# Performance work log

Hardware: AMD Instinct MI355X
Metric: run time of the kernel (lower is better)

## Reference

```python
import jax, jax.numpy as jnp
import numpy as np

H, C = 4, 32  # heads, per-head out_channels; hidden = H*C = 128


def _gatv2(x, Wl, bl, Wr, br, att, b, src, dst):
    """One PyG GATv2Conv layer (concat=True, add_self_loops=False, slope=0.2)."""
    N = x.shape[0]
    xl = (x @ Wl + bl).reshape(N, H, C)  # source transform (messages)
    xr = (x @ Wr + br).reshape(N, H, C)  # target transform
    msg = xl[src]                         # [E,H,C] gather per edge
    e = jax.nn.leaky_relu(msg + xr[dst], 0.2)
    a = jnp.einsum('ehc,hc->eh', e, att)  # [E,H] attention logits
    # segment softmax over incoming edges of each target node
    amax = jax.ops.segment_max(a, dst, num_segments=N)
    a = jnp.exp(a - amax[dst])
    denom = jax.ops.segment_sum(a, dst, num_segments=N)
    a = a / (denom[dst] + 1e-16)
    out = jax.ops.segment_sum(a[..., None] * msg, dst, num_segments=N)  # [N,H,C]
    return out.reshape(N, H * C) + b


def setup_inputs() -> dict:
    key = jax.random.key(0)
    ks = jax.random.split(key, 16)
    N, E, F = 50000, 800000, H * C
    s = 1.0 / np.sqrt(F)
    inp = {
        'x': jax.random.normal(ks[0], (N, F), dtype=jnp.float32),
        'edge_index': jax.random.randint(ks[1], (2, E), 0, N, dtype=jnp.int32),
    }
    names = ['Wl1', 'Wr1', 'Wl2', 'Wr2']
    for i, n in enumerate(names):
        inp[n] = jax.random.normal(ks[2 + i], (F, F), dtype=jnp.float32) * s
    inp['bl1'] = jnp.zeros((F,), jnp.float32)
    inp['br1'] = jnp.zeros((F,), jnp.float32)
    inp['bl2'] = jnp.zeros((F,), jnp.float32)
    inp['br2'] = jnp.zeros((F,), jnp.float32)
    inp['att1'] = jax.random.normal(ks[6], (H, C), dtype=jnp.float32) * s
    inp['att2'] = jax.random.normal(ks[7], (H, C), dtype=jnp.float32) * s
    inp['b1'] = jnp.zeros((F,), jnp.float32)
    inp['b2'] = jnp.zeros((F,), jnp.float32)
    return inp


def reference(x, edge_index, Wl1, bl1, Wr1, br1, att1, b1,
              Wl2, bl2, Wr2, br2, att2, b2):
    src, dst = edge_index[0], edge_index[1]
    h = jax.nn.relu(_gatv2(x, Wl1, bl1, Wr1, br1, att1, b1, src, dst))
    out = _gatv2(h, Wl2, bl2, Wr2, br2, att2, b2, src, dst)
    return out
```

## Files before the change

kernel.cpp:

```cpp
#include <hip/hip_runtime.h>
#include <hip/hip_bf16.h>
#include <hip/hip_fp16.h>
#include <float.h>

#define F 128
#define HEADS 4
#define CPH 32

#define NB 512
#define BSHIFT 7
#define G 64

using f16x8 = __attribute__((ext_vector_type(8))) _Float16;
using f32x4 = __attribute__((ext_vector_type(4))) float;


__global__ __launch_bounds__(1024) void bucket_hist_kernel(
    const int* __restrict__ dst, int* __restrict__ counts, int E, int chunk)
{
    __shared__ int hist[NB];
    int blk = blockIdx.x;
    for (int b = threadIdx.x; b < NB; b += 1024) hist[b] = 0;
    __syncthreads();
    int e0 = blk * chunk, e1 = min(e0 + chunk, E);
    for (int e = e0 + threadIdx.x; e < e1; e += 1024)
        atomicAdd(&hist[dst[e] >> BSHIFT], 1);
    __syncthreads();
    for (int b = threadIdx.x; b < NB; b += 1024)
        counts[b * G + blk] = hist[b];
}

__global__ __launch_bounds__(1024) void scan1_kernel(const int* __restrict__ in,
                                                     int* __restrict__ excl,
                                                     int* __restrict__ bsums, int n) {
    __shared__ int tmp[1024];
    int i = blockIdx.x * 1024 + threadIdx.x;
    int v = (i < n) ? in[i] : 0;
    tmp[threadIdx.x] = v;
    __syncthreads();
    for (int o = 1; o < 1024; o <<= 1) {
        int a = (threadIdx.x >= o) ? tmp[threadIdx.x - o] : 0;
        __syncthreads();
        tmp[threadIdx.x] += a;
        __syncthreads();
    }
    if (i < n) excl[i] = tmp[threadIdx.x] - v;
    if (threadIdx.x == 1023) bsums[blockIdx.x] = tmp[1023];
}

__global__ __launch_bounds__(1024) void scan2_kernel(int* __restrict__ bsums, int nb) {
    __shared__ int tmp[1024];
    int v = (threadIdx.x < nb) ? bsums[threadIdx.x] : 0;
    tmp[threadIdx.x] = v;
    __syncthreads();
    for (int o = 1; o < 1024; o <<= 1) {
        int a = (threadIdx.x >= o) ? tmp[threadIdx.x - o] : 0;
        __syncthreads();
        tmp[threadIdx.x] += a;
        __syncthreads();
    }
    if (threadIdx.x < nb) bsums[threadIdx.x] = tmp[threadIdx.x] - v;
}

__global__ __launch_bounds__(1024) void addback_kernel(const int* __restrict__ excl,
                                                       const int* __restrict__ bsums,
                                                       int* __restrict__ offsets, int n) {
    int i = blockIdx.x * 1024 + threadIdx.x;
    if (i < n) offsets[i] = excl[i] + bsums[i >> 10];
}

__global__ __launch_bounds__(1024) void bucket_scatter_kernel(
    const int* __restrict__ src, const int* __restrict__ dst,
    const int* __restrict__ offsets, uint2* __restrict__ pairs, int E, int chunk)
{
    __shared__ int curs[NB];
    int blk = blockIdx.x;
    for (int b = threadIdx.x; b < NB; b += 1024) curs[b] = offsets[b * G + blk];
    __syncthreads();
    int e0 = blk * chunk, e1 = min(e0 + chunk, E);
    for (int e = e0 + threadIdx.x; e < e1; e += 1024) {
        int d = dst[e];
        int pos = atomicAdd(&curs[d >> BSHIFT], 1);
        pairs[pos] = make_uint2((unsigned)src[e], (unsigned)d);
    }
}

__global__ __launch_bounds__(256) void bucket_csr_kernel(
    const uint2* __restrict__ pairs, const int* __restrict__ offsets,
    int* __restrict__ row_ptr, int* __restrict__ srcs, int N, int E)
{
    int b = blockIdx.x;
    int seg0 = offsets[b * G];
    int seg1 = (b < NB - 1) ? offsets[(b + 1) * G] : E;
    __shared__ int hist[128], curs[128];
    if (threadIdx.x < 128) hist[threadIdx.x] = 0;
    __syncthreads();
    for (int e = seg0 + threadIdx.x; e < seg1; e += 256)
        atomicAdd(&hist[pairs[e].y & 127], 1);
    __syncthreads();
    int v = (threadIdx.x < 128) ? hist[threadIdx.x] : 0;
    if (threadIdx.x < 128) curs[threadIdx.x] = v;
    __syncthreads();
    for (int o = 1; o < 128; o <<= 1) {
        int a = 0;
        if (threadIdx.x < 128 && threadIdx.x >= o) a = curs[threadIdx.x - o];
        __syncthreads();
        if (threadIdx.x < 128) curs[threadIdx.x] += a;
        __syncthreads();
    }
    int excl = (threadIdx.x < 128) ? curs[threadIdx.x] - v : 0;
    __syncthreads();
    if (threadIdx.x < 128) {
        int node = b * 128 + threadIdx.x;
        if (node <= N) row_ptr[node] = seg0 + excl;
        curs[threadIdx.x] = excl;
    }
    __syncthreads();
    for (int e = seg0 + threadIdx.x; e < seg1; e += 256) {
        uint2 p = pairs[e];
        int pos = seg0 + atomicAdd(&curs[p.y & 127], 1);
        srcs[pos] = (int)p.x;
    }
}

__global__ void convw_kernel(const float* __restrict__ W0, const float* __restrict__ W1,
                             const float* __restrict__ W2, const float* __restrict__ W3,
                             _Float16* __restrict__ T0, _Float16* __restrict__ T1,
                             _Float16* __restrict__ T2, _Float16* __restrict__ T3) {
    int m   = blockIdx.x >> 6;
    int tid = (blockIdx.x & 63) * 256 + threadIdx.x;
    int n = tid >> 7, k = tid & 127;
    const float* W = m == 0 ? W0 : m == 1 ? W1 : m == 2 ? W2 : W3;
    _Float16*    T = m == 0 ? T0 : m == 1 ? T1 : m == 2 ? T2 : T3;
    T[tid] = (_Float16)W[k * F + n];
}


template<int A_FP32>
__global__ __launch_bounds__(256) void mfma_gemm_kernel(
    const void* __restrict__ Xin,
    const _Float16* __restrict__ Wlt, const float* __restrict__ bl,
    const _Float16* __restrict__ Wrt, const float* __restrict__ br,
    _Float16* __restrict__ xl, float* __restrict__ xr, int N)
{
    const int m = blockIdx.y;
    const _Float16* Wt = m ? Wrt : Wlt;

    __shared__ f16x8 Ws[F * 17];
    for (int i = threadIdx.x; i < F * 16; i += 256) {
        int row = i >> 4, g = i & 15;
        Ws[row * 17 + g] = ((const f16x8*)Wt)[i];
    }
    __syncthreads();

    const int wid  = threadIdx.x >> 6;
    const int lane = threadIdx.x & 63;
    const int row0 = blockIdx.x * 64 + wid * 16;
    const int arow = lane & 15;
    const int g    = lane >> 4;

    int xrow = row0 + arow;
    if (xrow >= N) xrow = N - 1;
    f16x8 af[4];
    if (A_FP32) {
        const float* xp = (const float*)Xin + (size_t)xrow * F + g * 8;
        #pragma unroll
        for (int t = 0; t < 4; ++t) {
            float4 lo = *(const float4*)(xp + t * 32);
            float4 hi = *(const float4*)(xp + t * 32 + 4);
            f16x8 a;
            a[0] = (_Float16)lo.x; a[1] = (_Float16)lo.y; a[2] = (_Float16)lo.z; a[3] = (_Float16)lo.w;
            a[4] = (_Float16)hi.x; a[5] = (_Float16)hi.y; a[6] = (_Float16)hi.z; a[7] = (_Float16)hi.w;
            af[t] = a;
        }
    } else {
        const _Float16* xp = (const _Float16*)Xin + (size_t)xrow * F + g * 8;
        #pragma unroll
        for (int t = 0; t < 4; ++t)
            af[t] = *(const f16x8*)(xp + t * 32);
    }

    f32x4 acc[8];
    #pragma unroll
    for (int nt = 0; nt < 8; ++nt) acc[nt] = (f32x4){0.f, 0.f, 0.f, 0.f};

    #pragma unroll
    for (int t = 0; t < 4; ++t)
        #pragma unroll
        for (int nt = 0; nt < 8; ++nt) {
            f16x8 b = Ws[(nt * 16 + arow) * 17 + (t * 4 + g)];
            acc[nt] = __builtin_amdgcn_mfma_f32_16x16x32_f16(af[t], b, acc[nt], 0, 0, 0);
        }

    const float* bias = m ? br : bl;
    #pragma unroll
    for (int nt = 0; nt < 8; ++nt) {
        int ccol = nt * 16 + (lane & 15);
        float bv = bias[ccol];
        #pragma unroll
        for (int r2 = 0; r2 < 4; ++r2) {
            int crow = row0 + (lane >> 4) * 4 + r2;
            if (crow < N) {
                float v = acc[nt][r2] + bv;
                if (m == 0) xl[(size_t)crow * F + ccol] = (_Float16)v;
                else        xr[(size_t)crow * F + ccol] = v;
            }
        }
    }
}


__global__ __launch_bounds__(256) void gat_edge_kernel(
    const _Float16* __restrict__ xlh, const float* __restrict__ xr,
    const int* __restrict__ srcs, const int* __restrict__ row_ptr,
    const float* __restrict__ att, const float* __restrict__ bias,
    float* __restrict__ outf, _Float16* __restrict__ outh,
    int N, int do_relu, int out_half)
{
    int node = blockIdx.x * 4 + threadIdx.y;
    if (node >= N) return;
    int lane = threadIdx.x;
    int es = lane >> 4;
    int q  = lane & 15;

    const float* xrp = xr + (size_t)node * F + q * 8;
    float4 xa = *(const float4*)(xrp);
    float4 xb = *(const float4*)(xrp + 4);
    float xr8[8] = {xa.x, xa.y, xa.z, xa.w, xb.x, xb.y, xb.z, xb.w};
    float4 aa = *(const float4*)(att + q * 8);
    float4 ab = *(const float4*)(att + q * 8 + 4);
    float at8[8] = {aa.x, aa.y, aa.z, aa.w, ab.x, ab.y, ab.z, ab.w};

    int beg = row_ptr[node], end = row_ptr[node + 1];
    float s = 0.f;
    float o[8] = {0.f, 0.f, 0.f, 0.f, 0.f, 0.f, 0.f, 0.f};

    for (int i = beg; i < end; i += 8) {
        int iA = i + es;
        bool vA = iA < end;
        int snA = srcs[vA ? iA : beg];
        f16x8 hA = *(const f16x8*)(xlh + (size_t)snA * F + q * 8);
        int iB = i + 4 + es;
        bool vB = iB < end;
        int snB = srcs[vB ? iB : beg];
        f16x8 hB = *(const f16x8*)(xlh + (size_t)snB * F + q * 8);

        float a[8], b[8];
        #pragma unroll
        for (int j = 0; j < 8; ++j) { a[j] = (float)hA[j]; b[j] = (float)hB[j]; }

        float pA = 0.f, pB = 0.f;
        #pragma unroll
        for (int j = 0; j < 8; ++j) {
            float eA = a[j] + xr8[j];
            eA = fmaxf(eA, 0.2f * eA);
            pA = fmaf(eA, at8[j], pA);
            float eB = b[j] + xr8[j];
            eB = fmaxf(eB, 0.2f * eB);
            pB = fmaf(eB, at8[j], pB);
        }
        pA += __shfl_xor(pA, 1); pA += __shfl_xor(pA, 2);
        pB += __shfl_xor(pB, 1); pB += __shfl_xor(pB, 2);
        float wA = vA ? __expf(pA) : 0.f;
        float wB = vB ? __expf(pB) : 0.f;
        s += wA + wB;
        #pragma unroll
        for (int j = 0; j < 8; ++j) {
            o[j] = fmaf(wA, a[j], o[j]);
            o[j] = fmaf(wB, b[j], o[j]);
        }
    }

    s += __shfl_xor(s, 16); s += __shfl_xor(s, 32);
    #pragma unroll
    for (int j = 0; j < 8; ++j) {
        o[j] += __shfl_xor(o[j], 16);
        o[j] += __shfl_xor(o[j], 32);
    }

    if (es == 0) {
        float inv = 1.f / (s + 1e-16f);
        float r[8];
        #pragma unroll
        for (int j = 0; j < 8; ++j) {
            r[j] = fmaf(o[j], inv, bias[q * 8 + j]);
            if (do_relu) r[j] = fmaxf(r[j], 0.f);
        }
        if (out_half) {
            f16x8 hv;
            #pragma unroll
            for (int j = 0; j < 8; ++j) hv[j] = (_Float16)r[j];
            *(f16x8*)(outh + (size_t)node * F + q * 8) = hv;
        } else {
            float4 lo = {r[0], r[1], r[2], r[3]};
            float4 hi = {r[4], r[5], r[6], r[7]};
            *(float4*)(outf + (size_t)node * F + q * 8) = lo;
            *(float4*)(outf + (size_t)node * F + q * 8 + 4) = hi;
        }
    }
}


extern "C" void kernel_launch(void* const* d_in, const int* in_sizes, int n_in,
                              void* d_out, int out_size, void* d_ws, size_t ws_size,
                              hipStream_t stream)
{
    const float* x    = (const float*)d_in[0];
    const int*   ei   = (const int*)d_in[1];
    const float* Wl1  = (const float*)d_in[2];
    const float* Wr1  = (const float*)d_in[3];
    const float* Wl2  = (const float*)d_in[4];
    const float* Wr2  = (const float*)d_in[5];
    const float* bl1  = (const float*)d_in[6];
    const float* br1  = (const float*)d_in[7];
    const float* bl2  = (const float*)d_in[8];
    const float* br2  = (const float*)d_in[9];
    const float* att1 = (const float*)d_in[10];
    const float* att2 = (const float*)d_in[11];
    const float* b1   = (const float*)d_in[12];
    const float* b2   = (const float*)d_in[13];

    const int N = in_sizes[0] / F;
    const int E = in_sizes[1] / 2;
    const int* src = ei;
    const int* dst = ei + E;

    char* ws = (char*)d_ws;
    size_t off = 0;
    auto alloc = [&](size_t bytes) -> void* {
        void* p = ws + off;
        off = (off + bytes + 255) & ~(size_t)255;
        return p;
    };
    _Float16* hh   = (_Float16*)alloc((size_t)N * F * sizeof(_Float16));
    _Float16* xlh  = (_Float16*)alloc((size_t)N * F * sizeof(_Float16));
    float*    xr   = (float*)alloc((size_t)N * F * sizeof(float));
    _Float16* Wt1l = (_Float16*)alloc((size_t)F * F * sizeof(_Float16));
    _Float16* Wt1r = (_Float16*)alloc((size_t)F * F * sizeof(_Float16));
    _Float16* Wt2l = (_Float16*)alloc((size_t)F * F * sizeof(_Float16));
    _Float16* Wt2r = (_Float16*)alloc((size_t)F * F * sizeof(_Float16));
    int*   row_ptr = (int*)alloc((size_t)(N + 1) * sizeof(int));
    int*   counts  = (int*)alloc((size_t)NB * G * sizeof(int));
    int*   cexcl   = (int*)alloc((size_t)NB * G * sizeof(int));
    int*   bsums   = (int*)alloc((size_t)1024 * sizeof(int));
    int*   offsets = (int*)alloc((size_t)NB * G * sizeof(int));
    uint2* pairs   = (uint2*)alloc((size_t)E * sizeof(uint2));
    int*   srcs    = (int*)alloc((size_t)E * sizeof(int));

    const int chunk = (E + G - 1) / G;
    const int ncounts = NB * G;
    bucket_hist_kernel<<<G, 1024, 0, stream>>>(dst, counts, E, chunk);
    scan1_kernel<<<ncounts / 1024, 1024, 0, stream>>>(counts, cexcl, bsums, ncounts);
    scan2_kernel<<<1, 1024, 0, stream>>>(bsums, ncounts / 1024);
    addback_kernel<<<ncounts / 1024, 1024, 0, stream>>>(cexcl, bsums, offsets, ncounts);
    bucket_scatter_kernel<<<G, 1024, 0, stream>>>(src, dst, offsets, pairs, E, chunk);
    bucket_csr_kernel<<<NB, 256, 0, stream>>>(pairs, offsets, row_ptr, srcs, N, E);

    convw_kernel<<<256, 256, 0, stream>>>(Wl1, Wr1, Wl2, Wr2, Wt1l, Wt1r, Wt2l, Wt2r);

    const int gemm_blocks = (N + 63) / 64;
    dim3 gemm_grid(gemm_blocks, 2);
    dim3 eb(64, 4);
    const int edge_blocks = (N + 3) / 4;

    mfma_gemm_kernel<1><<<gemm_grid, 256, 0, stream>>>(
        x, Wt1l, bl1, Wt1r, br1, xlh, xr, N);
    gat_edge_kernel<<<edge_blocks, eb, 0, stream>>>(
        xlh, xr, srcs, row_ptr, att1, b1, nullptr, hh, N, 1, 1);

    mfma_gemm_kernel<0><<<gemm_grid, 256, 0, stream>>>(
        hh, Wt2l, bl2, Wt2r, br2, xlh, xr, N);
    gat_edge_kernel<<<edge_blocks, eb, 0, stream>>>(
        xlh, xr, srcs, row_ptr, att2, b2, (float*)d_out, nullptr, N, 0, 0);
}
```

Measured before the change: 175.6 us.

## Fuse preprocessing kernels and compute edge attention logits in packed fp16

Merges the weight conversion into the histogram kernel and collapses the three-kernel scan into one single-block scan, cutting kernel launches in the CSR build. The edge kernel now computes the leaky-relu attention dot product with packed half2 arithmetic instead of fp32 and unrolls the edge loop by two. The fp16 logit accumulation lowers precision and adds rounding risk before the exponent.

Result: faster. 167.6 us (-4.6%).

```diff
diff --git a/kernel.cpp b/kernel.cpp
--- a/kernel.cpp
+++ b/kernel.cpp
@@ -11,62 +11,61 @@
 #define BSHIFT 7
 #define G 64
 
+using f16x2 = __attribute__((ext_vector_type(2))) _Float16;
 using f16x8 = __attribute__((ext_vector_type(8))) _Float16;
 using f32x4 = __attribute__((ext_vector_type(4))) float;
 
 
-__global__ __launch_bounds__(1024) void bucket_hist_kernel(
-    const int* __restrict__ dst, int* __restrict__ counts, int E, int chunk)
+__global__ __launch_bounds__(1024) void hist_convw_kernel(
+    const int* __restrict__ dst, int* __restrict__ counts, int E, int chunk,
+    const float* __restrict__ W0, const float* __restrict__ W1,
+    const float* __restrict__ W2, const float* __restrict__ W3,
+    _Float16* __restrict__ T0, _Float16* __restrict__ T1,
+    _Float16* __restrict__ T2, _Float16* __restrict__ T3)
 {
     __shared__ int hist[NB];
-    int blk = blockIdx.x;
-    for (int b = threadIdx.x; b < NB; b += 1024) hist[b] = 0;
-    __syncthreads();
-    int e0 = blk * chunk, e1 = min(e0 + chunk, E);
-    for (int e = e0 + threadIdx.x; e < e1; e += 1024)
-        atomicAdd(&hist[dst[e] >> BSHIFT], 1);
-    __syncthreads();
-    for (int b = threadIdx.x; b < NB; b += 1024)
-        counts[b * G + blk] = hist[b];
-}
-
-__global__ __launch_bounds__(1024) void scan1_kernel(const int* __restrict__ in,
-                                                     int* __restrict__ excl,
-                                                     int* __restrict__ bsums, int n) {
+    if (blockIdx.x < G) {
+        int blk = blockIdx.x;
+        for (int b = threadIdx.x; b < NB; b += 1024) hist[b] = 0;
+        __syncthreads();
+        int e0 = blk * chunk, e1 = min(e0 + chunk, E);
+        for (int e = e0 + threadIdx.x; e < e1; e += 1024)
+            atomicAdd(&hist[dst[e] >> BSHIFT], 1);
+        __syncthreads();
+        for (int b = threadIdx.x; b < NB; b += 1024)
+            counts[b * G + blk] = hist[b];
+    } else {
+        int b = blockIdx.x - G;
+        int m = b >> 4;
+        int tid = (b & 15) * 1024 + threadIdx.x;
+        int n = tid >> 7, k = tid & 127;
+        const float* W = m == 0 ? W0 : m == 1 ? W1 : m == 2 ? W2 : W3;
+        _Float16*    T = m == 0 ? T0 : m == 1 ? T1 : m == 2 ? T2 : T3;
+        T[tid] = (_Float16)W[k * F + n];
+    }
+}
+
+
+__global__ __launch_bounds__(1024) void scan_fused_kernel(
+    const int* __restrict__ counts, int* __restrict__ offsets)
+{
     __shared__ int tmp[1024];
-    int i = blockIdx.x * 1024 + threadIdx.x;
-    int v = (i < n) ? in[i] : 0;
-    tmp[threadIdx.x] = v;
+    int t = threadIdx.x;
+    int loc[32];
+    int s = 0;
+    #pragma unroll
+    for (int j = 0; j < 32; ++j) { loc[j] = s; s += counts[t * 32 + j]; }
+    tmp[t] = s;
     __syncthreads();
     for (int o = 1; o < 1024; o <<= 1) {
-        int a = (threadIdx.x >= o) ? tmp[threadIdx.x - o] : 0;
-        __syncthreads();
-        tmp[threadIdx.x] += a;
-        __syncthreads();
-    }
-    if (i < n) excl[i] = tmp[threadIdx.x] - v;
-    if (threadIdx.x == 1023) bsums[blockIdx.x] = tmp[1023];
-}
-
-__global__ __launch_bounds__(1024) void scan2_kernel(int* __restrict__ bsums, int nb) {
-    __shared__ int tmp[1024];
-    int v = (threadIdx.x < nb) ? bsums[threadIdx.x] : 0;
-    tmp[threadIdx.x] = v;
-    __syncthreads();
-    for (int o = 1; o < 1024; o <<= 1) {
-        int a = (threadIdx.x >= o) ? tmp[threadIdx.x - o] : 0;
-        __syncthreads();
-        tmp[threadIdx.x] += a;
-        __syncthreads();
-    }
-    if (threadIdx.x < nb) bsums[threadIdx.x] = tmp[threadIdx.x] - v;
-}
-
-__global__ __launch_bounds__(1024) void addback_kernel(const int* __restrict__ excl,
-                                                       const int* __restrict__ bsums,
-                                                       int* __restrict__ offsets, int n) {
-    int i = blockIdx.x * 1024 + threadIdx.x;
-    if (i < n) offsets[i] = excl[i] + bsums[i >> 10];
+        int a = (t >= o) ? tmp[t - o] : 0;
+        __syncthreads();
+        tmp[t] += a;
+        __syncthreads();
+    }
+    int excl = tmp[t] - s;
+    #pragma unroll
+    for (int j = 0; j < 32; ++j) offsets[t * 32 + j] = excl + loc[j];
 }
 
 __global__ __launch_bounds__(1024) void bucket_scatter_kernel(
@@ -121,18 +120,6 @@
         int pos = seg0 + atomicAdd(&curs[p.y & 127], 1);
         srcs[pos] = (int)p.x;
     }
-}
-
-__global__ void convw_kernel(const float* __restrict__ W0, const float* __restrict__ W1,
-                             const float* __restrict__ W2, const float* __restrict__ W3,
-                             _Float16* __restrict__ T0, _Float16* __restrict__ T1,
-                             _Float16* __restrict__ T2, _Float16* __restrict__ T3) {
-    int m   = blockIdx.x >> 6;
-    int tid = (blockIdx.x & 63) * 256 + threadIdx.x;
-    int n = tid >> 7, k = tid & 127;
-    const float* W = m == 0 ? W0 : m == 1 ? W1 : m == 2 ? W2 : W3;
-    _Float16*    T = m == 0 ? T0 : m == 1 ? T1 : m == 2 ? T2 : T3;
-    T[tid] = (_Float16)W[k * F + n];
 }
 
 
@@ -226,39 +213,42 @@
     const float* xrp = xr + (size_t)node * F + q * 8;
     float4 xa = *(const float4*)(xrp);
     float4 xb = *(const float4*)(xrp + 4);
-    float xr8[8] = {xa.x, xa.y, xa.z, xa.w, xb.x, xb.y, xb.z, xb.w};
+    f16x2 xrh[4] = { {(_Float16)xa.x, (_Float16)xa.y}, {(_Float16)xa.z, (_Float16)xa.w},
+                     {(_Float16)xb.x, (_Float16)xb.y}, {(_Float16)xb.z, (_Float16)xb.w} };
     float4 aa = *(const float4*)(att + q * 8);
     float4 ab = *(const float4*)(att + q * 8 + 4);
-    float at8[8] = {aa.x, aa.y, aa.z, aa.w, ab.x, ab.y, ab.z, ab.w};
+    f16x2 ath[4] = { {(_Float16)aa.x, (_Float16)aa.y}, {(_Float16)aa.z, (_Float16)aa.w},
+                     {(_Float16)ab.x, (_Float16)ab.y}, {(_Float16)ab.z, (_Float16)ab.w} };
+    const f16x2 slope = {(_Float16)0.2f, (_Float16)0.2f};
 
     int beg = row_ptr[node], end = row_ptr[node + 1];
     float s = 0.f;
     float o[8] = {0.f, 0.f, 0.f, 0.f, 0.f, 0.f, 0.f, 0.f};
 
+    #pragma unroll 2
     for (int i = beg; i < end; i += 8) {
-        int iA = i + es;
-        bool vA = iA < end;
+        int iA = i + es;       bool vA = iA < end;
+        int iB = i + 4 + es;   bool vB = iB < end;
         int snA = srcs[vA ? iA : beg];
+        int snB = srcs[vB ? iB : beg];
         f16x8 hA = *(const f16x8*)(xlh + (size_t)snA * F + q * 8);
-        int iB = i + 4 + es;
-        bool vB = iB < end;
-        int snB = srcs[vB ? iB : beg];
         f16x8 hB = *(const f16x8*)(xlh + (size_t)snB * F + q * 8);
-
-        float a[8], b[8];
-        #pragma unroll
-        for (int j = 0; j < 8; ++j) { a[j] = (float)hA[j]; b[j] = (float)hB[j]; }
-
-        float pA = 0.f, pB = 0.f;
-        #pragma unroll
-        for (int j = 0; j < 8; ++j) {
-            float eA = a[j] + xr8[j];
-            eA = fmaxf(eA, 0.2f * eA);
-            pA = fmaf(eA, at8[j], pA);
-            float eB = b[j] + xr8[j];
-            eB = fmaxf(eB, 0.2f * eB);
-            pB = fmaf(eB, at8[j], pB);
-        }
+        const f16x2* a2 = (const f16x2*)&hA;
+        const f16x2* b2 = (const f16x2*)&hB;
+
+        f16x2 pA2 = {(_Float16)0.f, (_Float16)0.f};
+        f16x2 pB2 = {(_Float16)0.f, (_Float16)0.f};
+        #pragma unroll
+        for (int j = 0; j < 4; ++j) {
+            f16x2 eA = a2[j] + xrh[j];
+            eA = __builtin_elementwise_max(eA, eA * slope);
+            pA2 += eA * ath[j];
+            f16x2 eB = b2[j] + xrh[j];
+            eB = __builtin_elementwise_max(eB, eB * slope);
+            pB2 += eB * ath[j];
+        }
+        float pA = (float)pA2[0] + (float)pA2[1];
+        float pB = (float)pB2[0] + (float)pB2[1];
         pA += __shfl_xor(pA, 1); pA += __shfl_xor(pA, 2);
         pB += __shfl_xor(pB, 1); pB += __shfl_xor(pB, 2);
         float wA = vA ? __expf(pA) : 0.f;
@@ -266,8 +256,8 @@
         s += wA + wB;
         #pragma unroll
         for (int j = 0; j < 8; ++j) {
-            o[j] = fmaf(wA, a[j], o[j]);
-            o[j] = fmaf(wB, b[j], o[j]);
+            o[j] = fmaf(wA, (float)hA[j], o[j]);
+            o[j] = fmaf(wB, (float)hB[j], o[j]);
         }
     }
 
@@ -341,22 +331,17 @@
     _Float16* Wt2r = (_Float16*)alloc((size_t)F * F * sizeof(_Float16));
     int*   row_ptr = (int*)alloc((size_t)(N + 1) * sizeof(int));
     int*   counts  = (int*)alloc((size_t)NB * G * sizeof(int));
-    int*   cexcl   = (int*)alloc((size_t)NB * G * sizeof(int));
-    int*   bsums   = (int*)alloc((size_t)1024 * sizeof(int));
     int*   offsets = (int*)alloc((size_t)NB * G * sizeof(int));
     uint2* pairs   = (uint2*)alloc((size_t)E * sizeof(uint2));
     int*   srcs    = (int*)alloc((size_t)E * sizeof(int));
 
     const int chunk = (E + G - 1) / G;
-    const int ncounts = NB * G;
-    bucket_hist_kernel<<<G, 1024, 0, stream>>>(dst, counts, E, chunk);
-    scan1_kernel<<<ncounts / 1024, 1024, 0, stream>>>(counts, cexcl, bsums, ncounts);
-    scan2_kernel<<<1, 1024, 0, stream>>>(bsums, ncounts / 1024);
-    addback_kernel<<<ncounts / 1024, 1024, 0, stream>>>(cexcl, bsums, offsets, ncounts);
+    hist_convw_kernel<<<G + 64, 1024, 0, stream>>>(dst, counts, E, chunk,
+                                                   Wl1, Wr1, Wl2, Wr2,
+                                                   Wt1l, Wt1r, Wt2l, Wt2r);
+    scan_fused_kernel<<<1, 1024, 0, stream>>>(counts, offsets);
     bucket_scatter_kernel<<<G, 1024, 0, stream>>>(src, dst, offsets, pairs, E, chunk);
     bucket_csr_kernel<<<NB, 256, 0, stream>>>(pairs, offsets, row_ptr, srcs, N, E);
-
-    convw_kernel<<<256, 256, 0, stream>>>(Wl1, Wr1, Wl2, Wr2, Wt1l, Wt1r, Wt2l, Wt2r);
 
     const int gemm_blocks = (N + 63) / 64;
     dim3 gemm_grid(gemm_blocks, 2);
```
